# Optimization experiments

Measured on AMD Instinct MI355X. Metric: run time of the kernel, lower is better.

The kernel has to match this reference:

```python
import jax, jax.numpy as jnp
import numpy as np

MAX_LOGIT = 30.0
COV_WEIGHT = 1.0


def setup_inputs() -> dict:
    key = jax.random.key(0)
    ks = jax.random.split(key, 8)
    B, T, S, H = 8, 100, 400, 256
    sc = 1.0 / np.sqrt(H)
    return {
        "decoder_outputs": jax.random.normal(ks[0], (B, T, H), jnp.float32),
        "encoder_outputs": jax.random.normal(ks[1], (B, S, H), jnp.float32),
        "src_mask": jnp.zeros((B, S), dtype=bool),
        "W_h": jax.random.normal(ks[2], (H, H), jnp.float32) * sc,
        "W_s": jax.random.normal(ks[3], (H, H), jnp.float32) * sc,
        "w_c": jax.random.normal(ks[4], (H,), jnp.float32) * sc,  # Linear(1,H) weight
        "v": jax.random.normal(ks[5], (H,), jnp.float32) * sc,    # Linear(H,1) weight
        "b_attn": jnp.zeros((H,), jnp.float32),
    }


def reference(decoder_outputs, encoder_outputs, src_mask, W_h, W_s, w_c, v, b_attn):
    B, T, H = decoder_outputs.shape
    S = encoder_outputs.shape[1]
    neg_inf = jnp.float32(-jnp.inf)

    Wh = jnp.einsum('bsh,hk->bsk', encoder_outputs, W_h)   # [B,S,H]
    Ws = jnp.einsum('bth,hk->btk', decoder_outputs, W_s)   # [B,T,H]
    # E_base: [B,T,S,H]
    E_base = Wh[:, None, :, :] + Ws[:, :, None, :] + b_attn

    def logits(x):
        e = jnp.einsum('btsh,h->bts', jnp.tanh(x), v)
        e = jnp.clip(e, -MAX_LOGIT, MAX_LOGIT)
        return jnp.where(src_mask[:, None, :], neg_inf, e)

    A_prelim = jax.nn.softmax(logits(E_base), axis=-1)      # [B,T,S]
    cum = jnp.cumsum(A_prelim, axis=1)
    cov_shifted = jnp.concatenate(
        [jnp.zeros((B, 1, S), A_prelim.dtype), cum[:, :-1, :]], axis=1)  # [B,T,S]

    # W_c applied to scalar coverage: outer product with w_c -> [B,T,S,H]
    E_final = logits(E_base + cov_shifted[..., None] * w_c)
    A_final = jax.nn.softmax(E_final, axis=-1)              # [B,T,S]

    context = jnp.einsum('bts,bsh->bth', A_final, encoder_outputs)
    cov_loss = (COV_WEIGHT * jnp.sum(jnp.minimum(A_final, cov_shifted), axis=-1).mean())[None]
    return context, A_final, cov_loss
```

## Files before the change

kernel.cpp:

```cpp
#include <hip/hip_runtime.h>
#include <math.h>

#define B_ 8
#define T_ 100
#define S_ 400
#define H_ 256
#define BT_ (B_ * T_)
#define MAXL 30.0f
#define K_EXP 2.885390081777927f

#define AF_OFF (BT_ * H_)
#define LOSS_OFF (BT_ * H_ + BT_ * S_)

#define WHT_OFF 0
#define WSB_OFF (B_ * H_ * S_)
#define ACOV_OFF (WSB_OFF + BT_ * H_)

__device__ __forceinline__ float wave_sum(float p) {
#pragma unroll
    for (int off = 32; off; off >>= 1) p += __shfl_xor(p, off, 64);
    return p;
}

__device__ __forceinline__ float wave_max(float p) {
#pragma unroll
    for (int off = 32; off; off >>= 1) p = fmaxf(p, __shfl_xor(p, off, 64));
    return p;
}

#define ROWS 4
__global__ __launch_bounds__(256) void k_gemm(
    const float* __restrict__ dec, const float* __restrict__ enc,
    const float* __restrict__ W_h, const float* __restrict__ W_s,
    const float* __restrict__ b_attn,
    float* __restrict__ WhT, float* __restrict__ Wsb) {
    const int tid = threadIdx.x;
    const int blk = blockIdx.x;
    const int NB_ENC = (B_ * S_) / ROWS;

    float a0 = 0.f, a1 = 0.f, a2 = 0.f, a3 = 0.f;

    if (blk < NB_ENC) {
        const int r0 = blk * ROWS;
        const int b = r0 / S_, s0 = r0 - b * S_;
        const float* in = enc + (size_t)r0 * H_;
        const float* Wp = W_h + tid;
#pragma unroll 8
        for (int h = 0; h < H_; ++h) {
            float w = Wp[(size_t)h * H_];
            a0 = fmaf(in[h], w, a0);
            a1 = fmaf(in[H_ + h], w, a1);
            a2 = fmaf(in[2 * H_ + h], w, a2);
            a3 = fmaf(in[3 * H_ + h], w, a3);
        }
        float* o = WhT + ((size_t)b * H_ + tid) * S_ + s0;
        o[0] = K_EXP * a0;
        o[1] = K_EXP * a1;
        o[2] = K_EXP * a2;
        o[3] = K_EXP * a3;
    } else {
        const int bt0 = (blk - NB_ENC) * ROWS;
        const float* in = dec + (size_t)bt0 * H_;
        const float* Wp = W_s + tid;
        const float bias = b_attn[tid];
#pragma unroll 8
        for (int h = 0; h < H_; ++h) {
            float w = Wp[(size_t)h * H_];
            a0 = fmaf(in[h], w, a0);
            a1 = fmaf(in[H_ + h], w, a1);
            a2 = fmaf(in[2 * H_ + h], w, a2);
            a3 = fmaf(in[3 * H_ + h], w, a3);
        }
        Wsb[(size_t)(bt0 + 0) * H_ + tid] = K_EXP * (a0 + bias);
        Wsb[(size_t)(bt0 + 1) * H_ + tid] = K_EXP * (a1 + bias);
        Wsb[(size_t)(bt0 + 2) * H_ + tid] = K_EXP * (a2 + bias);
        Wsb[(size_t)(bt0 + 3) * H_ + tid] = K_EXP * (a3 + bias);
    }
}

__global__ __launch_bounds__(512) void k_prelim(
    const float* __restrict__ WhT, const float* __restrict__ Wsb,
    const float* __restrict__ v,
    const unsigned char* __restrict__ mask,
    float* __restrict__ A) {
    __shared__ float red[32];
    const int blk = blockIdx.x;
    const int b = blk & 7;
    const int tp = blk >> 3;
    const int bt0 = b * T_ + 2 * tp;
    const int tid = threadIdx.x;
    const int lane = tid & 63;
    const int wid = tid >> 6;
    const int s = tid;
    const bool act = (s < S_);

    const float4 vv4 = *reinterpret_cast<const float4*>(v + 4 * lane);
    const float sumv = wave_sum((vv4.x + vv4.y) + (vv4.z + vv4.w));

    const float* Ws0 = Wsb + (size_t)bt0 * H_;
    const float* Ws1 = Ws0 + H_;
    float acc0 = 0.f, acc1 = 0.f;
    if (act) {
        const float* wcol = WhT + (size_t)b * H_ * S_ + s;
#pragma unroll 8
        for (int h = 0; h < H_; ++h) {
            float w = wcol[(size_t)h * S_];
            float vh = v[h];
            float r0 = __builtin_amdgcn_rcpf(__builtin_amdgcn_exp2f(w + Ws0[h]) + 1.0f);
            float r1 = __builtin_amdgcn_rcpf(__builtin_amdgcn_exp2f(w + Ws1[h]) + 1.0f);
            acc0 = fmaf(r0, vh, acc0);
            acc1 = fmaf(r1, vh, acc1);
        }
    }

    float e0 = -INFINITY, e1 = -INFINITY;
    if (act) {
        e0 = fminf(fmaxf(sumv - 2.f * acc0, -MAXL), MAXL);
        e1 = fminf(fmaxf(sumv - 2.f * acc1, -MAXL), MAXL);
        if (mask[(size_t)b * S_ + s]) { e0 = -INFINITY; e1 = -INFINITY; }
    }

    float mx0 = wave_max(e0);
    float mx1 = wave_max(e1);
    if (lane == 0) { red[wid] = mx0; red[8 + wid] = mx1; }
    __syncthreads();
    mx0 = fmaxf(fmaxf(fmaxf(red[0], red[1]), fmaxf(red[2], red[3])),
                fmaxf(fmaxf(red[4], red[5]), fmaxf(red[6], red[7])));
    mx1 = fmaxf(fmaxf(fmaxf(red[8], red[9]), fmaxf(red[10], red[11])),
                fmaxf(fmaxf(red[12], red[13]), fmaxf(red[14], red[15])));

    float p0 = act ? __expf(e0 - mx0) : 0.f;
    float p1 = act ? __expf(e1 - mx1) : 0.f;
    float sm0 = wave_sum(p0);
    float sm1 = wave_sum(p1);
    if (lane == 0) { red[16 + wid] = sm0; red[24 + wid] = sm1; }
    __syncthreads();
    sm0 = ((red[16] + red[17]) + (red[18] + red[19])) +
          ((red[20] + red[21]) + (red[22] + red[23]));
    sm1 = ((red[24] + red[25]) + (red[26] + red[27])) +
          ((red[28] + red[29]) + (red[30] + red[31]));

    if (act) {
        A[(size_t)bt0 * S_ + s] = p0 * __builtin_amdgcn_rcpf(sm0);
        A[(size_t)(bt0 + 1) * S_ + s] = p1 * __builtin_amdgcn_rcpf(sm1);
    }
}

__global__ __launch_bounds__(64) void k_cumsum(float* __restrict__ A,
                                               float* __restrict__ out) {
    const int idx = blockIdx.x * 64 + threadIdx.x;
    if (idx == 0) out[LOSS_OFF] = 0.f;
    if (idx >= B_ * S_) return;
    const int b = idx / S_;
    const int s = idx - b * S_;
    float* col = A + (size_t)b * T_ * S_ + s;
    float run = 0.f;
#pragma unroll 10
    for (int t = 0; t < T_; ++t) {
        float a = col[(size_t)t * S_];
        col[(size_t)t * S_] = run;
        run += a;
    }
}

__global__ __launch_bounds__(512) void k_final(
    const float* __restrict__ WhT, const float* __restrict__ Wsb,
    const float* __restrict__ v, const float* __restrict__ w_c,
    const float* __restrict__ cov,
    const unsigned char* __restrict__ mask,
    const float* __restrict__ enc,
    float* __restrict__ out) {
    __shared__ float e0_lds[S_], e1_lds[S_];
    __shared__ float ctx0[H_], ctx1[H_];
    __shared__ float red[32];
    const int blk = blockIdx.x;
    const int b = blk & 7;
    const int tp = blk >> 3;
    const int bt0 = b * T_ + 2 * tp;
    const int tid = threadIdx.x;
    const int lane = tid & 63;
    const int wid = tid >> 6;
    const int s = tid;
    const bool act = (s < S_);

    const float4 vv4 = *reinterpret_cast<const float4*>(v + 4 * lane);
    const float sumv = wave_sum((vv4.x + vv4.y) + (vv4.z + vv4.w));

    float c0 = 0.f, c1 = 0.f;
    if (act) {
        c0 = cov[(size_t)bt0 * S_ + s];
        c1 = cov[(size_t)(bt0 + 1) * S_ + s];
    }
    const float ck0 = K_EXP * c0, ck1 = K_EXP * c1;

    const float* Ws0 = Wsb + (size_t)bt0 * H_;
    const float* Ws1 = Ws0 + H_;
    float acc0 = 0.f, acc1 = 0.f;
    if (act) {
        const float* wcol = WhT + (size_t)b * H_ * S_ + s;
#pragma unroll 8
        for (int h = 0; h < H_; ++h) {
            float w = wcol[(size_t)h * S_];
            float wch = w_c[h];
            float vh = v[h];
            float a0 = fmaf(ck0, wch, w + Ws0[h]);
            float a1 = fmaf(ck1, wch, w + Ws1[h]);
            float r0 = __builtin_amdgcn_rcpf(__builtin_amdgcn_exp2f(a0) + 1.0f);
            float r1 = __builtin_amdgcn_rcpf(__builtin_amdgcn_exp2f(a1) + 1.0f);
            acc0 = fmaf(r0, vh, acc0);
            acc1 = fmaf(r1, vh, acc1);
        }
    }

    float e0 = -INFINITY, e1 = -INFINITY;
    if (act) {
        e0 = fminf(fmaxf(sumv - 2.f * acc0, -MAXL), MAXL);
        e1 = fminf(fmaxf(sumv - 2.f * acc1, -MAXL), MAXL);
        if (mask[(size_t)b * S_ + s]) { e0 = -INFINITY; e1 = -INFINITY; }
    }

    float mx0 = wave_max(e0);
    float mx1 = wave_max(e1);
    if (lane == 0) { red[wid] = mx0; red[8 + wid] = mx1; }
    __syncthreads();
    mx0 = fmaxf(fmaxf(fmaxf(red[0], red[1]), fmaxf(red[2], red[3])),
                fmaxf(fmaxf(red[4], red[5]), fmaxf(red[6], red[7])));
    mx1 = fmaxf(fmaxf(fmaxf(red[8], red[9]), fmaxf(red[10], red[11])),
                fmaxf(fmaxf(red[12], red[13]), fmaxf(red[14], red[15])));

    float p0 = act ? __expf(e0 - mx0) : 0.f;
    float p1 = act ? __expf(e1 - mx1) : 0.f;
    float sm0 = wave_sum(p0);
    float sm1 = wave_sum(p1);
    if (lane == 0) { red[16 + wid] = sm0; red[24 + wid] = sm1; }
    __syncthreads();
    sm0 = ((red[16] + red[17]) + (red[18] + red[19])) +
          ((red[20] + red[21]) + (red[22] + red[23]));
    sm1 = ((red[24] + red[25]) + (red[26] + red[27])) +
          ((red[28] + red[29]) + (red[30] + red[31]));

    const float a0 = act ? p0 * __builtin_amdgcn_rcpf(sm0) : 0.f;
    const float a1 = act ? p1 * __builtin_amdgcn_rcpf(sm1) : 0.f;

    float lp = act ? (fminf(a0, c0) + fminf(a1, c1)) : 0.f;
    lp = wave_sum(lp);
    if (lane == 0) red[wid] = lp;

    if (act) {
        e0_lds[s] = a0;
        e1_lds[s] = a1;
        out[AF_OFF + (size_t)bt0 * S_ + s] = a0;
        out[AF_OFF + (size_t)(bt0 + 1) * S_ + s] = a1;
    }
    __syncthreads();

    if (tid == 0) {
        float tot = ((red[0] + red[1]) + (red[2] + red[3])) +
                    ((red[4] + red[5]) + (red[6] + red[7]));
        atomicAdd(out + LOSS_OFF, tot * (1.0f / (B_ * T_)));
    }

    const int h = tid & (H_ - 1);
    const int half = tid >> 8;
    const int sb = half * (S_ / 2);
    const float* eb = enc + ((size_t)b * S_ + sb) * H_ + h;
    float q00 = 0.f, q01 = 0.f, q02 = 0.f, q03 = 0.f;
    float q10 = 0.f, q11 = 0.f, q12 = 0.f, q13 = 0.f;
#pragma unroll 5
    for (int j = 0; j < S_ / 2; j += 4) {
        float w0 = eb[(size_t)j * H_];
        float w1 = eb[(size_t)(j + 1) * H_];
        float w2 = eb[(size_t)(j + 2) * H_];
        float w3 = eb[(size_t)(j + 3) * H_];
        q00 = fmaf(e0_lds[sb + j], w0, q00);
        q10 = fmaf(e1_lds[sb + j], w0, q10);
        q01 = fmaf(e0_lds[sb + j + 1], w1, q01);
        q11 = fmaf(e1_lds[sb + j + 1], w1, q11);
        q02 = fmaf(e0_lds[sb + j + 2], w2, q02);
        q12 = fmaf(e1_lds[sb + j + 2], w2, q12);
        q03 = fmaf(e0_lds[sb + j + 3], w3, q03);
        q13 = fmaf(e1_lds[sb + j + 3], w3, q13);
    }
    const float r0 = (q00 + q01) + (q02 + q03);
    const float r1 = (q10 + q11) + (q12 + q13);
    if (half == 0) { ctx0[h] = r0; ctx1[h] = r1; }
    __syncthreads();
    if (half == 1) {
        out[(size_t)bt0 * H_ + h] = ctx0[h] + r0;
        out[(size_t)(bt0 + 1) * H_ + h] = ctx1[h] + r1;
    }
}

extern "C" void kernel_launch(void* const* d_in, const int* in_sizes, int n_in,
                              void* d_out, int out_size, void* d_ws, size_t ws_size,
                              hipStream_t stream) {
    const float* dec = (const float*)d_in[0];
    const float* enc = (const float*)d_in[1];
    const unsigned char* mask = (const unsigned char*)d_in[2];
    const float* W_h = (const float*)d_in[3];
    const float* W_s = (const float*)d_in[4];
    const float* w_c = (const float*)d_in[5];
    const float* v = (const float*)d_in[6];
    const float* b_attn = (const float*)d_in[7];

    float* out = (float*)d_out;
    float* ws = (float*)d_ws;
    float* WhT = ws + WHT_OFF;
    float* Wsb = ws + WSB_OFF;
    float* Acov = ws + ACOV_OFF;

    const int nb_gemm = (B_ * S_) / ROWS + BT_ / ROWS;
    const int nb_pair = B_ * (T_ / 2);
    k_gemm<<<nb_gemm, 256, 0, stream>>>(dec, enc, W_h, W_s, b_attn, WhT, Wsb);
    k_prelim<<<nb_pair, 512, 0, stream>>>(WhT, Wsb, v, mask, Acov);
    k_cumsum<<<(B_ * S_ + 63) / 64, 64, 0, stream>>>(Acov, out);
    k_final<<<nb_pair, 512, 0, stream>>>(WhT, Wsb, v, w_c, Acov, mask, enc, out);
}
```

Before: 163.3 us.

## Factor exp of tanh argument into precomputed exponentials to remove inner-loop exp

The GEMM kernel now stores exp2 of the scaled projections, so the prelim kernel computes exp(a+b) as a product, 1/(1+Ea*Eb), with no transcendental exp in its inner loop. The final kernel still needs exp2 of the coverage term per h and pair, so it trades one exp per element for one exp plus extra multiplies. The GEMM also moves from 4 to 8 rows per block for more weight reuse. The product of exponentials can overflow to inf for large arguments; rcp(inf) gives 0, which is still the right limit, but precision behaviour changes.

```diff
diff --git a/kernel.cpp b/kernel.cpp
--- a/kernel.cpp
+++ b/kernel.cpp
@@ -12,9 +12,9 @@
 #define AF_OFF (BT_ * H_)
 #define LOSS_OFF (BT_ * H_ + BT_ * S_)
 
-#define WHT_OFF 0
-#define WSB_OFF (B_ * H_ * S_)
-#define ACOV_OFF (WSB_OFF + BT_ * H_)
+#define EWHT_OFF 0
+#define EWSB_OFF (B_ * H_ * S_)
+#define ACOV_OFF (EWSB_OFF + BT_ * H_)
 
 __device__ __forceinline__ float wave_sum(float p) {
 #pragma unroll
@@ -28,58 +28,57 @@
     return p;
 }
 
-#define ROWS 4
+#define ROWS 8
 __global__ __launch_bounds__(256) void k_gemm(
     const float* __restrict__ dec, const float* __restrict__ enc,
     const float* __restrict__ W_h, const float* __restrict__ W_s,
     const float* __restrict__ b_attn,
-    float* __restrict__ WhT, float* __restrict__ Wsb) {
+    float* __restrict__ EWhT, float* __restrict__ EWsb) {
     const int tid = threadIdx.x;
     const int blk = blockIdx.x;
     const int NB_ENC = (B_ * S_) / ROWS;
 
-    float a0 = 0.f, a1 = 0.f, a2 = 0.f, a3 = 0.f;
+    float acc[ROWS];
+#pragma unroll
+    for (int r = 0; r < ROWS; ++r) acc[r] = 0.f;
 
     if (blk < NB_ENC) {
         const int r0 = blk * ROWS;
         const int b = r0 / S_, s0 = r0 - b * S_;
         const float* in = enc + (size_t)r0 * H_;
         const float* Wp = W_h + tid;
-#pragma unroll 8
+#pragma unroll 4
         for (int h = 0; h < H_; ++h) {
             float w = Wp[(size_t)h * H_];
-            a0 = fmaf(in[h], w, a0);
-            a1 = fmaf(in[H_ + h], w, a1);
-            a2 = fmaf(in[2 * H_ + h], w, a2);
-            a3 = fmaf(in[3 * H_ + h], w, a3);
+#pragma unroll
+            for (int r = 0; r < ROWS; ++r)
+                acc[r] = fmaf(in[r * H_ + h], w, acc[r]);
         }
-        float* o = WhT + ((size_t)b * H_ + tid) * S_ + s0;
-        o[0] = K_EXP * a0;
-        o[1] = K_EXP * a1;
-        o[2] = K_EXP * a2;
-        o[3] = K_EXP * a3;
+        float* o = EWhT + ((size_t)b * H_ + tid) * S_ + s0;
+#pragma unroll
+        for (int r = 0; r < ROWS; ++r)
+            o[r] = __builtin_amdgcn_exp2f(K_EXP * acc[r]);
     } else {
         const int bt0 = (blk - NB_ENC) * ROWS;
         const float* in = dec + (size_t)bt0 * H_;
         const float* Wp = W_s + tid;
         const float bias = b_attn[tid];
-#pragma unroll 8
+#pragma unroll 4
         for (int h = 0; h < H_; ++h) {
             float w = Wp[(size_t)h * H_];
-            a0 = fmaf(in[h], w, a0);
-            a1 = fmaf(in[H_ + h], w, a1);
-            a2 = fmaf(in[2 * H_ + h], w, a2);
-            a3 = fmaf(in[3 * H_ + h], w, a3);
+#pragma unroll
+            for (int r = 0; r < ROWS; ++r)
+                acc[r] = fmaf(in[r * H_ + h], w, acc[r]);
         }
-        Wsb[(size_t)(bt0 + 0) * H_ + tid] = K_EXP * (a0 + bias);
-        Wsb[(size_t)(bt0 + 1) * H_ + tid] = K_EXP * (a1 + bias);
-        Wsb[(size_t)(bt0 + 2) * H_ + tid] = K_EXP * (a2 + bias);
-        Wsb[(size_t)(bt0 + 3) * H_ + tid] = K_EXP * (a3 + bias);
+#pragma unroll
+        for (int r = 0; r < ROWS; ++r)
+            EWsb[(size_t)(bt0 + r) * H_ + tid] =
+                __builtin_amdgcn_exp2f(K_EXP * (acc[r] + bias));
     }
 }
 
 __global__ __launch_bounds__(512) void k_prelim(
-    const float* __restrict__ WhT, const float* __restrict__ Wsb,
+    const float* __restrict__ EWhT, const float* __restrict__ EWsb,
     const float* __restrict__ v,
     const unsigned char* __restrict__ mask,
     float* __restrict__ A) {
@@ -97,17 +96,17 @@
     const float4 vv4 = *reinterpret_cast<const float4*>(v + 4 * lane);
     const float sumv = wave_sum((vv4.x + vv4.y) + (vv4.z + vv4.w));
 
-    const float* Ws0 = Wsb + (size_t)bt0 * H_;
-    const float* Ws1 = Ws0 + H_;
+    const float* E0 = EWsb + (size_t)bt0 * H_;
+    const float* E1 = E0 + H_;
     float acc0 = 0.f, acc1 = 0.f;
     if (act) {
-        const float* wcol = WhT + (size_t)b * H_ * S_ + s;
+        const float* ecol = EWhT + (size_t)b * H_ * S_ + s;
 #pragma unroll 8
         for (int h = 0; h < H_; ++h) {
-            float w = wcol[(size_t)h * S_];
+            float Ew = ecol[(size_t)h * S_];
             float vh = v[h];
-            float r0 = __builtin_amdgcn_rcpf(__builtin_amdgcn_exp2f(w + Ws0[h]) + 1.0f);
-            float r1 = __builtin_amdgcn_rcpf(__builtin_amdgcn_exp2f(w + Ws1[h]) + 1.0f);
+            float r0 = __builtin_amdgcn_rcpf(fmaf(Ew, E0[h], 1.0f));
+            float r1 = __builtin_amdgcn_rcpf(fmaf(Ew, E1[h], 1.0f));
             acc0 = fmaf(r0, vh, acc0);
             acc1 = fmaf(r1, vh, acc1);
         }
@@ -164,7 +163,7 @@
 }
 
 __global__ __launch_bounds__(512) void k_final(
-    const float* __restrict__ WhT, const float* __restrict__ Wsb,
+    const float* __restrict__ EWhT, const float* __restrict__ EWsb,
     const float* __restrict__ v, const float* __restrict__ w_c,
     const float* __restrict__ cov,
     const unsigned char* __restrict__ mask,
@@ -193,20 +192,20 @@
     }
     const float ck0 = K_EXP * c0, ck1 = K_EXP * c1;
 
-    const float* Ws0 = Wsb + (size_t)bt0 * H_;
-    const float* Ws1 = Ws0 + H_;
+    const float* E0 = EWsb + (size_t)bt0 * H_;
+    const float* E1 = E0 + H_;
     float acc0 = 0.f, acc1 = 0.f;
     if (act) {
-        const float* wcol = WhT + (size_t)b * H_ * S_ + s;
+        const float* ecol = EWhT + (size_t)b * H_ * S_ + s;
 #pragma unroll 8
         for (int h = 0; h < H_; ++h) {
-            float w = wcol[(size_t)h * S_];
+            float Ew = ecol[(size_t)h * S_];
             float wch = w_c[h];
             float vh = v[h];
-            float a0 = fmaf(ck0, wch, w + Ws0[h]);
-            float a1 = fmaf(ck1, wch, w + Ws1[h]);
-            float r0 = __builtin_amdgcn_rcpf(__builtin_amdgcn_exp2f(a0) + 1.0f);
-            float r1 = __builtin_amdgcn_rcpf(__builtin_amdgcn_exp2f(a1) + 1.0f);
+            float Ec0 = __builtin_amdgcn_exp2f(ck0 * wch);
+            float Ec1 = __builtin_amdgcn_exp2f(ck1 * wch);
+            float r0 = __builtin_amdgcn_rcpf(fmaf(Ew * E0[h], Ec0, 1.0f));
+            float r1 = __builtin_amdgcn_rcpf(fmaf(Ew * E1[h], Ec1, 1.0f));
             acc0 = fmaf(r0, vh, acc0);
             acc1 = fmaf(r1, vh, acc1);
         }
@@ -305,14 +304,14 @@
 
     float* out = (float*)d_out;
     float* ws = (float*)d_ws;
-    float* WhT = ws + WHT_OFF;
-    float* Wsb = ws + WSB_OFF;
+    float* EWhT = ws + EWHT_OFF;
+    float* EWsb = ws + EWSB_OFF;
     float* Acov = ws + ACOV_OFF;
 
     const int nb_gemm = (B_ * S_) / ROWS + BT_ / ROWS;
     const int nb_pair = B_ * (T_ / 2);
-    k_gemm<<<nb_gemm, 256, 0, stream>>>(dec, enc, W_h, W_s, b_attn, WhT, Wsb);
-    k_prelim<<<nb_pair, 512, 0, stream>>>(WhT, Wsb, v, mask, Acov);
+    k_gemm<<<nb_gemm, 256, 0, stream>>>(dec, enc, W_h, W_s, b_attn, EWhT, EWsb);
+    k_prelim<<<nb_pair, 512, 0, stream>>>(EWhT, EWsb, v, mask, Acov);
     k_cumsum<<<(B_ * S_ + 63) / 64, 64, 0, stream>>>(Acov, out);
-    k_final<<<nb_pair, 512, 0, stream>>>(WhT, Wsb, v, w_c, Acov, mask, enc, out);
-}
+    k_final<<<nb_pair, 512, 0, stream>>>(EWhT, EWsb, v, w_c, Acov, mask, enc, out);
+}
```

Result: no change. 162.2 us (-0.7%).
